# Kernel tuning notes

Hardware: AMD Instinct MI355X
Metric: run time of the kernel (lower is better)

Reference implementation:

```python
import jax, jax.numpy as jnp
import numpy as np

NUM_HEADS = 8


def _mab(Q, K, Wq, bq, Wk, bk, Wv, bv, Wo, bo):
    # MAB with ln=False, dropout=0 (eval). Scale is sqrt(dim_V), matching source.
    B, Lq, _ = Q.shape
    Lk = K.shape[1]
    Dv = Wq.shape[1]
    dh = Dv // NUM_HEADS
    q = (Q @ Wq + bq).reshape(B, Lq, NUM_HEADS, dh).transpose(0, 2, 1, 3)
    k = (K @ Wk + bk).reshape(B, Lk, NUM_HEADS, dh).transpose(0, 2, 1, 3)
    v = (K @ Wv + bv).reshape(B, Lk, NUM_HEADS, dh).transpose(0, 2, 1, 3)
    A = jax.nn.softmax(jnp.einsum('bhqd,bhkd->bhqk', q, k) / jnp.sqrt(jnp.float32(Dv)), axis=-1)
    O = (q + jnp.einsum('bhqk,bhkd->bhqd', A, v)).transpose(0, 2, 1, 3).reshape(B, Lq, Dv)
    return O + jax.nn.relu(O @ Wo + bo)


def _forward(x, adj, gin_W, gin_b, geW1, geb1, geW2, geb2,
             gnW1, gnb1, gnW2, gnb2, goW, gob, S,
             mWq, mbq, mWk, mbk, mWv, mbv, mWo, mbo, finW, finb):
    B, V, T, D = x.shape
    Hd = gin_W.shape[1]
    # --- GNN encoder (adj path) ---
    h = x.reshape(B, V, T * D) @ gin_W + gin_b            # [B,V,H]
    # edge_mlp first linear on cat([h_i,h_j]) == h@Wi (row) + h@Wj (col); avoids 2H concat
    Wi, Wj = geW1[:Hd], geW1[Hd:]
    pre = (h @ Wi)[:, :, None, :] + (h @ Wj)[:, None, :, :] + geb1   # [B,V,V,H]
    e = jax.nn.relu(jax.nn.relu(pre) @ geW2 + geb2)       # [B,V,V,H]
    agg = jnp.einsum('bijh,bij->bih', e, adj)             # mask * sum over j, fused
    node = jax.nn.relu(jax.nn.relu(agg @ gnW1 + gnb1) @ gnW2 + gnb2)
    enc = node @ goW + gob                                # [B,V,H]
    # --- decoder: PMA + SAB + SAB + Linear ---
    o = _mab(jnp.broadcast_to(S, (B,) + S.shape[1:]), enc,
             mWq[0], mbq[0], mWk[0], mbk[0], mWv[0], mbv[0], mWo[0], mbo[0])
    o = _mab(o, o, mWq[1], mbq[1], mWk[1], mbk[1], mWv[1], mbv[1], mWo[1], mbo[1])
    o = _mab(o, o, mWq[2], mbq[2], mWk[2], mbk[2], mWv[2], mbv[2], mWo[2], mbo[2])
    out = o @ finW + finb                                 # [B,num_slots,T*OD]
    return out.reshape(B, S.shape[1], T, finW.shape[1] // T)


def setup_inputs() -> dict:
    key = jax.random.key(0)
    ks = jax.random.split(key, 16)
    B, V, T, D = 4, 256, 12, 4
    H, NS, OD = 256, 16, 32

    def w(k, shape, s=0.02):
        return s * jax.random.normal(k, shape, jnp.float32)

    return {
        'x': jax.random.normal(ks[0], (B, V, T, D), jnp.float32),
        'adj': (jax.random.uniform(ks[1], (B, V, V)) > 0.5).astype(jnp.float32),
        'gin_W': w(ks[2], (T * D, H)), 'gin_b': jnp.zeros((H,), jnp.float32),
        'geW1': w(ks[3], (2 * H, H)), 'geb1': jnp.zeros((H,), jnp.float32),
        'geW2': w(ks[4], (H, H)), 'geb2': jnp.zeros((H,), jnp.float32),
        'gnW1': w(ks[5], (H, H)), 'gnb1': jnp.zeros((H,), jnp.float32),
        'gnW2': w(ks[6], (H, H)), 'gnb2': jnp.zeros((H,), jnp.float32),
        'goW': w(ks[7], (H, H)), 'gob': jnp.zeros((H,), jnp.float32),
        'S': w(ks[8], (1, NS, H), 0.05),
        'mWq': w(ks[9], (3, H, H)), 'mbq': jnp.zeros((3, H), jnp.float32),
        'mWk': w(ks[10], (3, H, H)), 'mbk': jnp.zeros((3, H), jnp.float32),
        'mWv': w(ks[11], (3, H, H)), 'mbv': jnp.zeros((3, H), jnp.float32),
        'mWo': w(ks[12], (3, H, H)), 'mbo': jnp.zeros((3, H), jnp.float32),
        'finW': w(ks[13], (H, T * OD)), 'finb': jnp.zeros((T * OD,), jnp.float32),
    }


def reference(x, adj, gin_W, gin_b, geW1, geb1, geW2, geb2,
              gnW1, gnb1, gnW2, gnb2, goW, gob, S,
              mWq, mbq, mWk, mbk, mWv, mbv, mWo, mbo, finW, finb):
    return _forward(x, adj, gin_W, gin_b, geW1, geb1, geW2, geb2,
                    gnW1, gnb1, gnW2, gnb2, goW, gob, S,
                    mWq, mbq, mWk, mbk, mWv, mbv, mWo, mbo, finW, finb)
```

## Files before the change

kernel.cpp:

```cpp
#include <hip/hip_runtime.h>
#include <hip/hip_bf16.h>

typedef unsigned short u16;
typedef __bf16 bf8v __attribute__((ext_vector_type(8)));
typedef float f4v __attribute__((ext_vector_type(4)));

__device__ __forceinline__ float b2f(u16 v) {
  union { unsigned u; float f; } x; x.u = ((unsigned)v) << 16; return x.f;
}
__device__ __forceinline__ u16 f2b(float f) {
  union { float f; unsigned u; } x; x.f = f;
  unsigned r = (x.u + 0x7FFFu + ((x.u >> 16) & 1u)) >> 16;
  return (u16)r;
}
__device__ __forceinline__ unsigned pkbf(float a, float b) {
  union { __hip_bfloat162 h; unsigned u; } c;
  c.h = __float22bfloat162_rn(make_float2(a, b));
  return c.u;
}
__device__ __forceinline__ void up2(unsigned u, float& lo, float& hi) {
  union { unsigned x; float f; } a, b;
  a.x = u << 16; b.x = u & 0xffff0000u; lo = a.f; hi = b.f;
}

#define NFRAG 19
struct PreArgs {
  const float* fsrc[NFRAG];
  u16* fdst[NFRAG];
  int fstride[NFRAG];
  int fbase[NFRAG + 1];
  int fragTiles, hBase, prepBid, q1Bid;
  const float *x, *ginW, *ginb;
  u16* h_bf;
  const float *mbk, *mbv, *mbq, *S, *mWq;
  float *bkv0, *bqkv1, *bqkv2;
  u16* q1b;
};

__global__ __launch_bounds__(256) void k_pre(PreArgs a) {
  __shared__ u16 ld[256 * 20];
  __shared__ float xs[4][48];
  __shared__ float Ss[4096];
  const int bid = blockIdx.x, t = threadIdx.x;

  if (bid < a.fragTiles) {
    int j = 0;
    while (j + 1 < NFRAG && a.fbase[j + 1] <= bid) j++;
    const int localT = bid - a.fbase[j];
    const float* src = a.fsrc[j];
    const int Ns = a.fstride[j];
    const int n0 = localT * 16;
    {
      const float* s = src + (size_t)t * Ns + n0;
      const float4 v0 = ((const float4*)s)[0], v1 = ((const float4*)s)[1];
      const float4 v2 = ((const float4*)s)[2], v3 = ((const float4*)s)[3];
      unsigned* row = (unsigned*)(ld + t * 20);
      row[0] = pkbf(v0.x, v0.y); row[1] = pkbf(v0.z, v0.w);
      row[2] = pkbf(v1.x, v1.y); row[3] = pkbf(v1.z, v1.w);
      row[4] = pkbf(v2.x, v2.y); row[5] = pkbf(v2.z, v2.w);
      row[6] = pkbf(v3.x, v3.y); row[7] = pkbf(v3.z, v3.w);
    }
    __syncthreads();
    u16* dst = a.fdst[j] + (size_t)localT * 4096;
#pragma unroll
    for (int s2 = 0; s2 < 2; s2++) {
      const int o = t * 2 + s2, kt = o >> 6, lane = o & 63;
      const int nlo = lane & 15, bk = kt * 32 + ((lane >> 4) << 3);
      union { u16 h[8]; uint4 q; } pk;
#pragma unroll
      for (int j2 = 0; j2 < 8; j2++) pk.h[j2] = ld[(bk + j2) * 20 + nlo];
      *(uint4*)(dst + (size_t)(kt * 64 + lane) * 8) = pk.q;
    }
    return;
  }
  if (bid >= a.hBase && bid < a.hBase + 256) {
    const int row0 = (bid - a.hBase) * 4;
    if (t < 192) {
      const int rr = t / 48, k = t % 48;
      xs[rr][k] = a.x[(size_t)(row0 + rr) * 48 + k];
    }
    __syncthreads();
    const float bias = a.ginb[t];
    float acc[4] = {bias, bias, bias, bias};
    for (int k = 0; k < 48; k++) {
      const float w = a.ginW[(size_t)k * 256 + t];
#pragma unroll
      for (int rr = 0; rr < 4; rr++) acc[rr] += xs[rr][k] * w;
    }
#pragma unroll
    for (int rr = 0; rr < 4; rr++) a.h_bf[(size_t)(row0 + rr) * 256 + t] = f2b(acc[rr]);
    return;
  }
  if (bid == a.prepBid) {
    a.bkv0[t] = a.mbk[t]; a.bkv0[256 + t] = a.mbv[t];
    a.bqkv1[t] = a.mbq[256 + t]; a.bqkv1[256 + t] = a.mbk[256 + t]; a.bqkv1[512 + t] = a.mbv[256 + t];
    a.bqkv2[t] = a.mbq[512 + t]; a.bqkv2[256 + t] = a.mbk[512 + t]; a.bqkv2[512 + t] = a.mbv[512 + t];
    return;
  }
  if (bid == a.q1Bid) {
    for (int idx = t; idx < 4096; idx += 256) Ss[idx] = a.S[idx];
    __syncthreads();
    float acc[16];
#pragma unroll
    for (int r = 0; r < 16; r++) acc[r] = 0.f;
    for (int k = 0; k < 256; k++) {
      const float w = a.mWq[(size_t)k * 256 + t];
#pragma unroll
      for (int r = 0; r < 16; r++) acc[r] += Ss[r * 256 + k] * w;
    }
    const float bq = a.mbq[t];
#pragma unroll
    for (int r = 0; r < 16; r++) a.q1b[r * 256 + t] = f2b(acc[r] + bq);
    return;
  }
}

__global__ __launch_bounds__(256) void k_wiwj(
    const u16* __restrict__ h, const u16* __restrict__ frag,
    float* __restrict__ hWiF, u16* __restrict__ hWjB) {
  __shared__ __align__(16) u16 As[64 * 264];
  const int t = threadIdx.x, lane = t & 63, wv = t >> 6;
  const int m0 = blockIdx.x * 64, n0 = blockIdx.y * 128;
  {
    const int row = t >> 2, ch = t & 3;
#pragma unroll
    for (int s = 0; s < 8; s++)
      *(uint4*)(As + row * 264 + ch * 64 + s * 8) =
          *(const uint4*)(h + (size_t)(m0 + row) * 256 + ch * 64 + s * 8);
  }
  __syncthreads();
  f4v acc[4][2];
#pragma unroll
// ... 120 lines not shown
      if (kt < 7) {
#pragma unroll
        for (int nt = 0; nt < 4; nt++) bcur[nt] = bnxt[nt];
      }
    }
    const int rbase = (lane >> 4) * 4;
#pragma unroll
    for (int nt = 0; nt < 4; nt++) {
      float s = 0.f;
#pragma unroll
      for (int jt = 0; jt < 4; jt++) {
        const int r0 = jt * 16 + rbase;
#pragma unroll
        for (int r = 0; r < 4; r++) {
          const float e = fmaxf(acc[jt][nt][r] + bias2[nt], 0.f);
          s += (r0 + r < rows) ? e : 0.f;
        }
      }
      s += __shfl_xor(s, 16);
      s += __shfl_xor(s, 32);
      aggAcc[nt] += s;
    }
    __syncthreads();
  }
  if (lane < 16) {
#pragma unroll
    for (int nt = 0; nt < 4; nt++) {
      const int n = wv * 64 + nt * 16 + lane;
      aggB[(size_t)(b * 256 + i) * 256 + n] = f2b(aggAcc[nt]);
    }
  }
}

#define NBLK 32

__device__ __forceinline__ void gridbar(int* cnt, int gen) {
  __syncthreads();
  if (threadIdx.x == 0) {
    __threadfence();
    __hip_atomic_fetch_add(cnt, 1, __ATOMIC_RELAXED, __HIP_MEMORY_SCOPE_AGENT);
    int it = 0;
    while (__hip_atomic_load(cnt, __ATOMIC_RELAXED, __HIP_MEMORY_SCOPE_AGENT) < NBLK * gen) {
      __builtin_amdgcn_s_sleep(8);
      if (((++it) & 255) == 0)
        __hip_atomic_fetch_add(cnt, 0, __ATOMIC_RELAXED, __HIP_MEMORY_SCOPE_AGENT);
    }
    __threadfence();
  }
  __syncthreads();
}

__device__ void g32(const u16* Al, const u16* frag, const float* bias, int relu,
                    u16* Ol, int t) {
  const int lane = t & 63, wv = t >> 6;
  f4v acc[2][4];
#pragma unroll
  for (int mt = 0; mt < 2; mt++)
#pragma unroll
    for (int nt = 0; nt < 4; nt++) acc[mt][nt] = (f4v){0.f, 0.f, 0.f, 0.f};
#pragma unroll
  for (int kt = 0; kt < 8; kt++) {
    bf8v af[2], bf[4];
#pragma unroll
    for (int mt = 0; mt < 2; mt++)
      af[mt] = *(const bf8v*)(Al + (mt * 16 + (lane & 15)) * 264 + kt * 32 + ((lane >> 4) << 3));
#pragma unroll
    for (int nt = 0; nt < 4; nt++)
      bf[nt] = *(const bf8v*)(frag + ((size_t)((wv * 4 + nt) * 8 + kt) * 64 + lane) * 8);
#pragma unroll
    for (int mt = 0; mt < 2; mt++)
#pragma unroll
      for (int nt = 0; nt < 4; nt++)
        acc[mt][nt] = __builtin_amdgcn_mfma_f32_16x16x32_bf16(af[mt], bf[nt], acc[mt][nt], 0, 0, 0);
  }
#pragma unroll
  for (int mt = 0; mt < 2; mt++)
#pragma unroll
    for (int nt = 0; nt < 4; nt++) {
      const int col = wv * 64 + nt * 16 + (lane & 15);
      const float bv = bias[col];
#pragma unroll
      for (int r = 0; r < 4; r++) {
        const int row = mt * 16 + ((lane >> 4) << 2) + r;
        float v = acc[mt][nt][r] + bv;
// ... 87 lines not shown
#pragma unroll
    for (int q2 = 0; q2 < 4; q2++) { v[q2] = __expf(v[q2] - mx); sum += v[q2]; }
    for (int off = 32; off; off >>= 1) sum += __shfl_xor(sum, off);
    const float inv = 1.f / sum;
#pragma unroll
    for (int q2 = 0; q2 < 4; q2++) sc[r * 256 + lane + q2 * 64] = v[q2] * inv;
  }
  __syncthreads();
  for (int u = t; u < 1024; u += 256) {
    const int row = u >> 2, part = u & 3;
    const uint4 v4 = *(const uint4*)(vbuf + (size_t)(b * Lk + row) * 512 + hd * 32 + part * 8);
    float f0, f1, f2, f3, f4, f5, f6, f7;
    up2(v4.x, f0, f1); up2(v4.y, f2, f3); up2(v4.z, f4, f5); up2(v4.w, f6, f7);
    float4* d = (float4*)(vs + row * 32 + part * 8);
    d[0] = make_float4(f0, f1, f2, f3);
    d[1] = make_float4(f4, f5, f6, f7);
  }
  __syncthreads();
  const int r0 = t >> 5, d = t & 31;
  float a0 = qs[r0 * 32 + d], a1 = qs[(r0 + 8) * 32 + d];
#pragma unroll 4
  for (int j = 0; j < Lk; j++) {
    const float vv = vs[j * 32 + d];
    a0 += sc[r0 * 256 + j] * vv;
    a1 += sc[(r0 + 8) * 256 + j] * vv;
  }
  const int c0 = hd * 32 + d;
  oF[(size_t)(b * 16 + r0) * 256 + c0] = a0;
  oB[(size_t)(b * 16 + r0) * 256 + c0] = f2b(a0);
  oF[(size_t)(b * 16 + r0 + 8) * 256 + c0] = a1;
  oB[(size_t)(b * 16 + r0 + 8) * 256 + c0] = f2b(a1);
}

__device__ void wprojG(const u16* __restrict__ o1b, const float* __restrict__ o1f,
                       const u16* __restrict__ frag, const float* __restrict__ bias,
                       u16* actL, float* residL, int b, int T, int lane) {
  f4v acc = (f4v){0.f, 0.f, 0.f, 0.f};
  const u16* abase = o1b + (size_t)(b * 16 + (lane & 15)) * 256 + ((lane >> 4) << 3);
  const u16* fbase = frag + ((size_t)(T * 8) * 64 + lane) * 8;
#pragma unroll
  for (int kt = 0; kt < 8; kt++)
    acc = __builtin_amdgcn_mfma_f32_16x16x32_bf16(*(const bf8v*)(abase + kt * 32),
                                                  *(const bf8v*)(fbase + (size_t)kt * 512), acc, 0, 0, 0);
  const int col = T * 16 + (lane & 15);
  const float bv = bias[col];
#pragma unroll
  for (int r = 0; r < 4; r++) {
    const int row = ((lane >> 4) << 2) + r;
    const float v = fmaxf(acc[r] + bv, 0.f) + o1f[(size_t)(b * 16 + row) * 256 + col];
    residL[row * 256 + col] = v;
    actL[row * 264 + col] = f2b(v);
  }
}

__device__ void wprojQ(const u16* actL, const u16* __restrict__ frag,
                       const float* __restrict__ bias, u16* qkvL, int T, int lane) {
  f4v acc = (f4v){0.f, 0.f, 0.f, 0.f};
  const u16* abase = actL + (lane & 15) * 264 + ((lane >> 4) << 3);
  const u16* fbase = frag + ((size_t)(T * 8) * 64 + lane) * 8;
#pragma unroll
  for (int kt = 0; kt < 8; kt++)
    acc = __builtin_amdgcn_mfma_f32_16x16x32_bf16(*(const bf8v*)(abase + kt * 32),
                                                  *(const bf8v*)(fbase + (size_t)kt * 512), acc, 0, 0, 0);
  const int col = T * 16 + (lane & 15);
  const float bv = bias[col];
#pragma unroll
  for (int r = 0; r < 4; r++) {
    const int row = ((lane >> 4) << 2) + r;
    qkvL[row * 776 + col] = f2b(acc[r] + bv);
  }
}

__device__ void wprojR(const u16* actIn, const u16* __restrict__ frag,
                       const float* __restrict__ bias, u16* actOut, float* residL,
                       int T, int lane) {
  f4v acc = (f4v){0.f, 0.f, 0.f, 0.f};
  const u16* abase = actIn + (lane & 15) * 264 + ((lane >> 4) << 3);
  const u16* fbase = frag + ((size_t)(T * 8) * 64 + lane) * 8;
#pragma unroll
  for (int kt = 0; kt < 8; kt++)
    acc = __builtin_amdgcn_mfma_f32_16x16x32_bf16(*(const bf8v*)(abase + kt * 32),
                                                  *(const bf8v*)(fbase + (size_t)kt * 512), acc, 0, 0, 0);
  const int col = T * 16 + (lane & 15);
  const float bv = bias[col];
#pragma unroll
  for (int r = 0; r < 4; r++) {
    const int row = ((lane >> 4) << 2) + r;
    const float v = fmaxf(acc[r] + bv, 0.f) + residL[row * 256 + col];
    residL[row * 256 + col] = v;
    actOut[row * 264 + col] = f2b(v);
  }
}

__device__ void wprojF(const u16* actL, const u16* __restrict__ frag,
                       const float* __restrict__ bias, float* __restrict__ outG,
                       int T, int lane) {
  f4v acc = (f4v){0.f, 0.f, 0.f, 0.f};
  const u16* abase = actL + (lane & 15) * 264 + ((lane >> 4) << 3);
  const u16* fbase = frag + ((size_t)(T * 8) * 64 + lane) * 8;
#pragma unroll
  for (int kt = 0; kt < 8; kt++)
    acc = __builtin_amdgcn_mfma_f32_16x16x32_bf16(*(const bf8v*)(abase + kt * 32),
                                                  *(const bf8v*)(fbase + (size_t)kt * 512), acc, 0, 0, 0);
  const int col = T * 16 + (lane & 15);
  const float bv = bias[col];
#pragma unroll
  for (int r = 0; r < 4; r++) {
    const int row = ((lane >> 4) << 2) + r;
    outG[(size_t)row * 384 + col] = acc[r] + bv;
  }
}

__device__ void attnB(const u16* qkvL, float* residL, u16* actOut, float* ps,
                      int hd, int lane) {
  const int r = lane & 15, cg = lane >> 4;
  float qv[32];
  {
    const uint4* qp = (const uint4*)(qkvL + r * 776 + hd * 32);
#pragma unroll
    for (int c4 = 0; c4 < 4; c4++) {
      const uint4 q4 = qp[c4];
      up2(q4.x, qv[c4 * 8 + 0], qv[c4 * 8 + 1]);
      up2(q4.y, qv[c4 * 8 + 2], qv[c4 * 8 + 3]);
      up2(q4.z, qv[c4 * 8 + 4], qv[c4 * 8 + 5]);
      up2(q4.w, qv[c4 * 8 + 6], qv[c4 * 8 + 7]);
    }
  }
  float p[4];
#pragma unroll
  for (int c = 0; c < 4; c++) {
    const int cc = cg * 4 + c;
    const uint4* kp = (const uint4*)(qkvL + cc * 776 + 256 + hd * 32);
    float s = 0.f;
#pragma unroll
    for (int c4 = 0; c4 < 4; c4++) {
      const uint4 k4 = kp[c4];
      float k0, k1;
      up2(k4.x, k0, k1); s += qv[c4 * 8 + 0] * k0 + qv[c4 * 8 + 1] * k1;
      up2(k4.y, k0, k1); s += qv[c4 * 8 + 2] * k0 + qv[c4 * 8 + 3] * k1;
      up2(k4.z, k0, k1); s += qv[c4 * 8 + 4] * k0 + qv[c4 * 8 + 5] * k1;
      up2(k4.w, k0, k1); s += qv[c4 * 8 + 6] * k0 + qv[c4 * 8 + 7] * k1;
    }
    p[c] = s * 0.0625f;
  }
  float mx = fmaxf(fmaxf(p[0], p[1]), fmaxf(p[2], p[3]));
  mx = fmaxf(mx, __shfl_xor(mx, 16));
  mx = fmaxf(mx, __shfl_xor(mx, 32));
  float sum = 0.f;
#pragma unroll
  for (int c = 0; c < 4; c++) { p[c] = __expf(p[c] - mx); sum += p[c]; }
  sum += __shfl_xor(sum, 16);
  sum += __shfl_xor(sum, 32);
  const float inv = 1.f / sum;
#pragma unroll
  for (int c = 0; c < 4; c++) ps[r * 16 + cg * 4 + c] = p[c] * inv;
  float o[8];
#pragma unroll
  for (int j = 0; j < 8; j++) o[j] = qv[cg * 8 + j];
#pragma unroll
  for (int c = 0; c < 16; c++) {
    const float pv = ps[r * 16 + c];
    const uint4 v4 = *(const uint4*)(qkvL + c * 776 + 512 + hd * 32 + cg * 8);
    float v0, v1;
    up2(v4.x, v0, v1); o[0] += pv * v0; o[1] += pv * v1;
    up2(v4.y, v0, v1); o[2] += pv * v0; o[3] += pv * v1;
    up2(v4.z, v0, v1); o[4] += pv * v0; o[5] += pv * v1;
    up2(v4.w, v0, v1); o[6] += pv * v0; o[7] += pv * v1;
  }
  const int col0 = hd * 32 + cg * 8;
#pragma unroll
  for (int j = 0; j < 8; j++) residL[r * 256 + col0 + j] = o[j];
  unsigned* ob = (unsigned*)(actOut + r * 264 + col0);
  ob[0] = pkbf(o[0], o[1]); ob[1] = pkbf(o[2], o[3]);
  ob[2] = pkbf(o[4], o[5]); ob[3] = pkbf(o[6], o[7]);
}

struct TailArgs {
  const u16 *agg, *fGn1, *fGn2, *fGo, *fKV0, *fQKV1, *fQKV2, *fO0, *fO1, *fO2, *fFin, *q1b;
  const float *gnb1, *gnb2, *gob, *bkv0, *bqkv1, *bqkv2, *mbo, *finb;
  u16 *kv1, *o1b;
  float *o1f, *outF;
  int* bar;
};

__global__ __launch_bounds__(256) void k_tail(TailArgs a) {
  __shared__ __align__(16) char smem[62208];
  const int bid = blockIdx.x, t = threadIdx.x;
  const int lane = t & 63, w = t >> 6;

  {
    u16* actA = (u16*)smem;
    u16* actB = (u16*)(smem + 16896);
    const int r0 = bid * 32;
#pragma unroll
    for (int s = 0; s < 4; s++) {
      const int u = t * 4 + s, row = u >> 5, ch = u & 31;
      *(uint4*)(actA + row * 264 + ch * 8) =
          *(const uint4*)(a.agg + (size_t)(r0 + row) * 256 + ch * 8);
    }
    __syncthreads();
    g32(actA, a.fGn1, a.gnb1, 1, actB, t); __syncthreads();
    g32(actB, a.fGn2, a.gnb2, 1, actA, t); __syncthreads();
    g32(actA, a.fGo, a.gob, 0, actB, t); __syncthreads();
    g32kv(actB, a.fKV0, a.bkv0, a.kv1 + (size_t)r0 * 512, t);
  }
  gridbar(a.bar, 1);
  {
    float* qs = (float*)smem;
    float* sc = (float*)(smem + 2048);
    float* vs = (float*)(smem + 18432);
    attn_tile(a.q1b, a.kv1, a.kv1 + 256, a.o1f, a.o1b, bid >> 3, bid & 7, qs, sc, vs, t);
  }
  gridbar(a.bar, 2);
  if (bid >= 4) return;
  {
    const int b = bid;
    u16* act0 = (u16*)smem;
    u16* act1 = (u16*)(smem + 8448);
    u16* qkvL = (u16*)(smem + 16896);
    float* residL = (float*)(smem + 41728);
    float* psL = (float*)(smem + 58112);
    __syncthreads();
    for (int T = w; T < 16; T += 4) wprojG(a.o1b, a.o1f, a.fO0, a.mbo, act0, residL, b, T, lane);
    __syncthreads();
    for (int T = w; T < 48; T += 4) wprojQ(act0, a.fQKV1, a.bqkv1, qkvL, T, lane);
    __syncthreads();
    for (int hd = w; hd < 8; hd += 4) attnB(qkvL, residL, act1, psL + w * 256, hd, lane);
    __syncthreads();
    for (int T = w; T < 16; T += 4) wprojR(act1, a.fO1, a.mbo + 256, act0, residL, T, lane);
    __syncthreads();
    for (int T = w; T < 48; T += 4) wprojQ(act0, a.fQKV2, a.bqkv2, qkvL, T, lane);
    __syncthreads();
    for (int hd = w; hd < 8; hd += 4) attnB(qkvL, residL, act1, psL + w * 256, hd, lane);
    __syncthreads();
    for (int T = w; T < 16; T += 4) wprojR(act1, a.fO2, a.mbo + 512, act0, residL, T, lane);
    __syncthreads();
    for (int T = w; T < 24; T += 4)
      wprojF(act0, a.fFin, a.finb, a.outF + (size_t)b * 16 * 384, T, lane);
  }
}

extern "C" void kernel_launch(void* const* d_in, const int* in_sizes, int n_in,
                              void* d_out, int out_size, void* d_ws, size_t ws_size,
                              hipStream_t stream) {
  const float* x    = (const float*)d_in[0];
  const float* adj  = (const float*)d_in[1];
  const float* ginW = (const float*)d_in[2];
  const float* ginb = (const float*)d_in[3];
  const float* geW1 = (const float*)d_in[4];
  const float* geb1 = (const float*)d_in[5];
  const float* geW2 = (const float*)d_in[6];
  const float* geb2 = (const float*)d_in[7];
  const float* gnW1 = (const float*)d_in[8];
  const float* gnb1 = (const float*)d_in[9];
  const float* gnW2 = (const float*)d_in[10];
  const float* gnb2 = (const float*)d_in[11];
  const float* goW  = (const float*)d_in[12];
  const float* gob  = (const float*)d_in[13];
  const float* S    = (const float*)d_in[14];
  const float* mWq  = (const float*)d_in[15];
  const float* mbq  = (const float*)d_in[16];
  const float* mWk  = (const float*)d_in[17];
  const float* mbk  = (const float*)d_in[18];
  const float* mWv  = (const float*)d_in[19];
  const float* mbv  = (const float*)d_in[20];
  const float* mWo  = (const float*)d_in[21];
  const float* mbo  = (const float*)d_in[22];
  const float* finW = (const float*)d_in[23];
  const float* finb = (const float*)d_in[24];
  (void)in_sizes; (void)n_in; (void)out_size; (void)ws_size;

  char* wp = (char*)d_ws;
  size_t off = 0;
  auto alloc = [&](size_t bytes) -> char* {
    char* p = wp + off;
    off += (bytes + 255) & ~(size_t)255;
    return p;
  };
  u16* h_bf     = (u16*)alloc(1024 * 256 * 2);
  float* hWiF   = (float*)alloc((size_t)1024 * 256 * 4);
  u16* hWjB     = (u16*)alloc(1024 * 256 * 2);
  u16* fWiWj    = (u16*)alloc(512 * 256 * 2);
  u16* fW2      = (u16*)alloc(256 * 256 * 2);
  u16* fGn1     = (u16*)alloc(256 * 256 * 2);
  u16* fGn2     = (u16*)alloc(256 * 256 * 2);
  u16* fGo      = (u16*)alloc(256 * 256 * 2);
  u16* fQ0      = (u16*)alloc(256 * 256 * 2);
  u16* fKV0     = (u16*)alloc(512 * 256 * 2);
  u16* fQKV1    = (u16*)alloc(768 * 256 * 2);
  u16* fQKV2    = (u16*)alloc(768 * 256 * 2);
  u16* fO0      = (u16*)alloc(256 * 256 * 2);
  u16* fO1      = (u16*)alloc(256 * 256 * 2);
  u16* fO2      = (u16*)alloc(256 * 256 * 2);
  u16* fFin     = (u16*)alloc(384 * 256 * 2);
  float* bkv0   = (float*)alloc(512 * 4);
  float* bqkv1  = (float*)alloc(768 * 4);
  float* bqkv2  = (float*)alloc(768 * 4);
  u16* q1b      = (u16*)alloc(16 * 256 * 2);
  u16* agg_b    = (u16*)alloc(1024 * 256 * 2);
  u16* kv1      = (u16*)alloc(1024 * 512 * 2);
  float* o1f    = (float*)alloc(64 * 256 * 4);
  u16* o1b      = (u16*)alloc(64 * 256 * 2);
  int* bar      = (int*)alloc(256);

  PreArgs P{};
  int nj = 0, tiles = 0;
  auto addF = [&](const float* s, int stride, u16* d, int nT) {
    P.fsrc[nj] = s; P.fdst[nj] = d; P.fstride[nj] = stride; P.fbase[nj] = tiles;
    tiles += nT; nj++;
  };
  addF(geW1, 256, fWiWj, 16);
  addF(geW1 + 65536, 256, fWiWj + 16 * 4096, 16);
  addF(geW2, 256, fW2, 16);
  addF(gnW1, 256, fGn1, 16);
  addF(gnW2, 256, fGn2, 16);
  addF(goW, 256, fGo, 16);
  addF(mWq, 256, fQ0, 16);
  addF(mWk, 256, fKV0, 16);
  addF(mWv, 256, fKV0 + 16 * 4096, 16);
  addF(mWq + 65536, 256, fQKV1, 16);
  addF(mWk + 65536, 256, fQKV1 + 16 * 4096, 16);
  addF(mWv + 65536, 256, fQKV1 + 32 * 4096, 16);
  addF(mWq + 131072, 256, fQKV2, 16);
  addF(mWk + 131072, 256, fQKV2 + 16 * 4096, 16);
  addF(mWv + 131072, 256, fQKV2 + 32 * 4096, 16);
  addF(mWo, 256, fO0, 16);
  addF(mWo + 65536, 256, fO1, 16);
  addF(mWo + 131072, 256, fO2, 16);
  addF(finW, 384, fFin, 24);
  P.fbase[nj] = tiles;
  P.fragTiles = tiles;
  P.hBase = tiles;
  P.prepBid = tiles + 256;
  P.q1Bid = tiles + 257;
  P.x = x; P.ginW = ginW; P.ginb = ginb; P.h_bf = h_bf;
  P.mbk = mbk; P.mbv = mbv; P.mbq = mbq; P.S = S; P.mWq = mWq;
  P.bkv0 = bkv0; P.bqkv1 = bqkv1; P.bqkv2 = bqkv2; P.q1b = q1b;

  TailArgs T{};
  T.agg = agg_b; T.fGn1 = fGn1; T.fGn2 = fGn2; T.fGo = fGo; T.fKV0 = fKV0;
  T.fQKV1 = fQKV1; T.fQKV2 = fQKV2; T.fO0 = fO0; T.fO1 = fO1; T.fO2 = fO2;
  T.fFin = fFin; T.q1b = q1b;
  T.gnb1 = gnb1; T.gnb2 = gnb2; T.gob = gob;
  T.bkv0 = bkv0; T.bqkv1 = bqkv1; T.bqkv2 = bqkv2; T.mbo = mbo; T.finb = finb;
  T.kv1 = kv1; T.o1b = o1b; T.o1f = o1f; T.outF = (float*)d_out;
  T.bar = bar;

  hipMemsetAsync(bar, 0, 256, stream);
  k_pre<<<dim3(tiles + 258), dim3(256), 0, stream>>>(P);
  k_wiwj<<<dim3(16, 4), dim3(256), 0, stream>>>(h_bf, fWiWj, hWiF, hWjB);
  k_edge<<<dim3(1024), dim3(256), 0, stream>>>(hWiF, hWjB, adj, geb1, fW2, geb2, agg_b);
  k_tail<<<dim3(NBLK), dim3(256), 0, stream>>>(T);
}
```

Measured before the change: 244.1 us.

## Split tail kernel at grid barriers into three launches and widen decoder blocks

New measurement: 248.9 us. About the same (+2.0%).

```diff
diff --git a/kernel.cpp b/kernel.cpp
--- a/kernel.cpp
+++ b/kernel.cpp
@@ -286,22 +286,6 @@
 
 #define NBLK 32
 
-__device__ __forceinline__ void gridbar(int* cnt, int gen) {
-  __syncthreads();
-  if (threadIdx.x == 0) {
-    __threadfence();
-    __hip_atomic_fetch_add(cnt, 1, __ATOMIC_RELAXED, __HIP_MEMORY_SCOPE_AGENT);
-    int it = 0;
-    while (__hip_atomic_load(cnt, __ATOMIC_RELAXED, __HIP_MEMORY_SCOPE_AGENT) < NBLK * gen) {
-      __builtin_amdgcn_s_sleep(8);
-      if (((++it) & 255) == 0)
-        __hip_atomic_fetch_add(cnt, 0, __ATOMIC_RELAXED, __HIP_MEMORY_SCOPE_AGENT);
-    }
-    __threadfence();
-  }
-  __syncthreads();
-}
-
 __device__ void g32(const u16* Al, const u16* frag, const float* bias, int relu,
                     u16* Ol, int t) {
   const int lane = t & 63, wv = t >> 6;
@@ -455,82 +439,125 @@
   oB[(size_t)(b * 16 + r0 + 8) * 256 + c0] = f2b(a1);
 }
 
-__device__ void wprojG(const u16* __restrict__ o1b, const float* __restrict__ o1f,
-                       const u16* __restrict__ frag, const float* __restrict__ bias,
-                       u16* actL, float* residL, int b, int T, int lane) {
-  f4v acc = (f4v){0.f, 0.f, 0.f, 0.f};
+
+template <int NT>
+__device__ __forceinline__ void wprojGn(
+    const u16* __restrict__ o1b, const float* __restrict__ o1f,
+    const u16* __restrict__ frag, const float* __restrict__ bias,
+    u16* actL, float* residL, int b, int T0, int lane) {
+  f4v acc[NT];
+#pragma unroll
+  for (int nt = 0; nt < NT; nt++) acc[nt] = (f4v){0.f, 0.f, 0.f, 0.f};
   const u16* abase = o1b + (size_t)(b * 16 + (lane & 15)) * 256 + ((lane >> 4) << 3);
-  const u16* fbase = frag + ((size_t)(T * 8) * 64 + lane) * 8;
-#pragma unroll
-  for (int kt = 0; kt < 8; kt++)
-    acc = __builtin_amdgcn_mfma_f32_16x16x32_bf16(*(const bf8v*)(abase + kt * 32),
-                                                  *(const bf8v*)(fbase + (size_t)kt * 512), acc, 0, 0, 0);
-  const int col = T * 16 + (lane & 15);
-  const float bv = bias[col];
-#pragma unroll
-  for (int r = 0; r < 4; r++) {
-    const int row = ((lane >> 4) << 2) + r;
-    const float v = fmaxf(acc[r] + bv, 0.f) + o1f[(size_t)(b * 16 + row) * 256 + col];
-    residL[row * 256 + col] = v;
-    actL[row * 264 + col] = f2b(v);
-  }
-}
-
-__device__ void wprojQ(const u16* actL, const u16* __restrict__ frag,
-                       const float* __restrict__ bias, u16* qkvL, int T, int lane) {
-  f4v acc = (f4v){0.f, 0.f, 0.f, 0.f};
+#pragma unroll
+  for (int kt = 0; kt < 8; kt++) {
+    const bf8v af = *(const bf8v*)(abase + kt * 32);
+#pragma unroll
+    for (int nt = 0; nt < NT; nt++) {
+      const bf8v bf = *(const bf8v*)(frag + ((size_t)((T0 + nt) * 8 + kt) * 64 + lane) * 8);
+      acc[nt] = __builtin_amdgcn_mfma_f32_16x16x32_bf16(af, bf, acc[nt], 0, 0, 0);
+    }
+  }
+#pragma unroll
+  for (int nt = 0; nt < NT; nt++) {
+    const int col = (T0 + nt) * 16 + (lane & 15);
+    const float bv = bias[col];
+#pragma unroll
+    for (int r = 0; r < 4; r++) {
+      const int row = ((lane >> 4) << 2) + r;
+      const float v = fmaxf(acc[nt][r] + bv, 0.f) + o1f[(size_t)(b * 16 + row) * 256 + col];
+      residL[row * 256 + col] = v;
+      actL[row * 264 + col] = f2b(v);
+    }
+  }
+}
+
+template <int NT>
+__device__ __forceinline__ void wprojQn(
+    const u16* actL, const u16* __restrict__ frag,
+    const float* __restrict__ bias, u16* qkvL, int T0, int lane) {
+  f4v acc[NT];
+#pragma unroll
+  for (int nt = 0; nt < NT; nt++) acc[nt] = (f4v){0.f, 0.f, 0.f, 0.f};
   const u16* abase = actL + (lane & 15) * 264 + ((lane >> 4) << 3);
-  const u16* fbase = frag + ((size_t)(T * 8) * 64 + lane) * 8;
-#pragma unroll
-  for (int kt = 0; kt < 8; kt++)
-    acc = __builtin_amdgcn_mfma_f32_16x16x32_bf16(*(const bf8v*)(abase + kt * 32),
-                                                  *(const bf8v*)(fbase + (size_t)kt * 512), acc, 0, 0, 0);
-  const int col = T * 16 + (lane & 15);
-  const float bv = bias[col];
-#pragma unroll
-  for (int r = 0; r < 4; r++) {
-    const int row = ((lane >> 4) << 2) + r;
-    qkvL[row * 776 + col] = f2b(acc[r] + bv);
-  }
-}
-
-__device__ void wprojR(const u16* actIn, const u16* __restrict__ frag,
-                       const float* __restrict__ bias, u16* actOut, float* residL,
-                       int T, int lane) {
-  f4v acc = (f4v){0.f, 0.f, 0.f, 0.f};
+#pragma unroll
+  for (int kt = 0; kt < 8; kt++) {
+    const bf8v af = *(const bf8v*)(abase + kt * 32);
+#pragma unroll
+    for (int nt = 0; nt < NT; nt++) {
+      const bf8v bf = *(const bf8v*)(frag + ((size_t)((T0 + nt) * 8 + kt) * 64 + lane) * 8);
+      acc[nt] = __builtin_amdgcn_mfma_f32_16x16x32_bf16(af, bf, acc[nt], 0, 0, 0);
+    }
+  }
+#pragma unroll
+  for (int nt = 0; nt < NT; nt++) {
+    const int col = (T0 + nt) * 16 + (lane & 15);
+    const float bv = bias[col];
+#pragma unroll
+    for (int r = 0; r < 4; r++) {
+      const int row = ((lane >> 4) << 2) + r;
+      qkvL[row * 776 + col] = f2b(acc[nt][r] + bv);
+    }
+  }
+}
+
+template <int NT>
+__device__ __forceinline__ void wprojRn(
+    const u16* actIn, const u16* __restrict__ frag,
+    const float* __restrict__ bias, u16* actOut, float* residL, int T0, int lane) {
+  f4v acc[NT];
+#pragma unroll
+  for (int nt = 0; nt < NT; nt++) acc[nt] = (f4v){0.f, 0.f, 0.f, 0.f};
   const u16* abase = actIn + (lane & 15) * 264 + ((lane >> 4) << 3);
-  const u16* fbase = frag + ((size_t)(T * 8) * 64 + lane) * 8;
-#pragma unroll
-  for (int kt = 0; kt < 8; kt++)
-    acc = __builtin_amdgcn_mfma_f32_16x16x32_bf16(*(const bf8v*)(abase + kt * 32),
-                                                  *(const bf8v*)(fbase + (size_t)kt * 512), acc, 0, 0, 0);
-  const int col = T * 16 + (lane & 15);
-  const float bv = bias[col];
-#pragma unroll
-  for (int r = 0; r < 4; r++) {
-    const int row = ((lane >> 4) << 2) + r;
-    const float v = fmaxf(acc[r] + bv, 0.f) + residL[row * 256 + col];
-    residL[row * 256 + col] = v;
-    actOut[row * 264 + col] = f2b(v);
-  }
-}
-
-__device__ void wprojF(const u16* actL, const u16* __restrict__ frag,
-                       const float* __restrict__ bias, float* __restrict__ outG,
-                       int T, int lane) {
-  f4v acc = (f4v){0.f, 0.f, 0.f, 0.f};
+#pragma unroll
+  for (int kt = 0; kt < 8; kt++) {
+    const bf8v af = *(const bf8v*)(abase + kt * 32);
+#pragma unroll
+    for (int nt = 0; nt < NT; nt++) {
+      const bf8v bf = *(const bf8v*)(frag + ((size_t)((T0 + nt) * 8 + kt) * 64 + lane) * 8);
+      acc[nt] = __builtin_amdgcn_mfma_f32_16x16x32_bf16(af, bf, acc[nt], 0, 0, 0);
+    }
+  }
+#pragma unroll
+  for (int nt = 0; nt < NT; nt++) {
+    const int col = (T0 + nt) * 16 + (lane & 15);
+    const float bv = bias[col];
+#pragma unroll
+    for (int r = 0; r < 4; r++) {
+      const int row = ((lane >> 4) << 2) + r;
+      const float v = fmaxf(acc[nt][r] + bv, 0.f) + residL[row * 256 + col];
+      residL[row * 256 + col] = v;
+      actOut[row * 264 + col] = f2b(v);
+    }
+  }
+}
+
+template <int NT>
+__device__ __forceinline__ void wprojFn(
+    const u16* actL, const u16* __restrict__ frag,
+    const float* __restrict__ bias, float* __restrict__ outG, int T0, int lane) {
+  f4v acc[NT];
+#pragma unroll
+  for (int nt = 0; nt < NT; nt++) acc[nt] = (f4v){0.f, 0.f, 0.f, 0.f};
   const u16* abase = actL + (lane & 15) * 264 + ((lane >> 4) << 3);
-  const u16* fbase = frag + ((size_t)(T * 8) * 64 + lane) * 8;
-#pragma unroll
-  for (int kt = 0; kt < 8; kt++)
-    acc = __builtin_amdgcn_mfma_f32_16x16x32_bf16(*(const bf8v*)(abase + kt * 32),
-                                                  *(const bf8v*)(fbase + (size_t)kt * 512), acc, 0, 0, 0);
-  const int col = T * 16 + (lane & 15);
-  const float bv = bias[col];
-#pragma unroll
-  for (int r = 0; r < 4; r++) {
-    const int row = ((lane >> 4) << 2) + r;
-    outG[(size_t)row * 384 + col] = acc[r] + bv;
+#pragma unroll
+  for (int kt = 0; kt < 8; kt++) {
+    const bf8v af = *(const bf8v*)(abase + kt * 32);
+#pragma unroll
+    for (int nt = 0; nt < NT; nt++) {
+      const bf8v bf = *(const bf8v*)(frag + ((size_t)((T0 + nt) * 8 + kt) * 64 + lane) * 8);
+      acc[nt] = __builtin_amdgcn_mfma_f32_16x16x32_bf16(af, bf, acc[nt], 0, 0, 0);
+    }
+  }
+#pragma unroll
+  for (int nt = 0; nt < NT; nt++) {
+    const int col = (T0 + nt) * 16 + (lane & 15);
+    const float bv = bias[col];
+#pragma unroll
+    for (int r = 0; r < 4; r++) {
+      const int row = ((lane >> 4) << 2) + r;
+      outG[(size_t)row * 384 + col] = acc[nt][r] + bv;
+    }
   }
 }
 
@@ -603,64 +630,61 @@
   const float *gnb1, *gnb2, *gob, *bkv0, *bqkv1, *bqkv2, *mbo, *finb;
   u16 *kv1, *o1b;
   float *o1f, *outF;
-  int* bar;
 };
 
-__global__ __launch_bounds__(256) void k_tail(TailArgs a) {
-  __shared__ __align__(16) char smem[62208];
+__global__ __launch_bounds__(256) void k_tail1(TailArgs a) {
+  __shared__ __align__(16) char smem[33792];
   const int bid = blockIdx.x, t = threadIdx.x;
-  const int lane = t & 63, w = t >> 6;
-
-  {
-    u16* actA = (u16*)smem;
-    u16* actB = (u16*)(smem + 16896);
-    const int r0 = bid * 32;
-#pragma unroll
-    for (int s = 0; s < 4; s++) {
-      const int u = t * 4 + s, row = u >> 5, ch = u & 31;
-      *(uint4*)(actA + row * 264 + ch * 8) =
-          *(const uint4*)(a.agg + (size_t)(r0 + row) * 256 + ch * 8);
-    }
-    __syncthreads();
-    g32(actA, a.fGn1, a.gnb1, 1, actB, t); __syncthreads();
-    g32(actB, a.fGn2, a.gnb2, 1, actA, t); __syncthreads();
-    g32(actA, a.fGo, a.gob, 0, actB, t); __syncthreads();
-    g32kv(actB, a.fKV0, a.bkv0, a.kv1 + (size_t)r0 * 512, t);
-  }
-  gridbar(a.bar, 1);
-  {
-    float* qs = (float*)smem;
-    float* sc = (float*)(smem + 2048);
-    float* vs = (float*)(smem + 18432);
-    attn_tile(a.q1b, a.kv1, a.kv1 + 256, a.o1f, a.o1b, bid >> 3, bid & 7, qs, sc, vs, t);
-  }
-  gridbar(a.bar, 2);
-  if (bid >= 4) return;
-  {
-    const int b = bid;
-    u16* act0 = (u16*)smem;
-    u16* act1 = (u16*)(smem + 8448);
-    u16* qkvL = (u16*)(smem + 16896);
-    float* residL = (float*)(smem + 41728);
-    float* psL = (float*)(smem + 58112);
-    __syncthreads();
-    for (int T = w; T < 16; T += 4) wprojG(a.o1b, a.o1f, a.fO0, a.mbo, act0, residL, b, T, lane);
-    __syncthreads();
-    for (int T = w; T < 48; T += 4) wprojQ(act0, a.fQKV1, a.bqkv1, qkvL, T, lane);
-    __syncthreads();
-    for (int hd = w; hd < 8; hd += 4) attnB(qkvL, residL, act1, psL + w * 256, hd, lane);
-    __syncthreads();
-    for (int T = w; T < 16; T += 4) wprojR(act1, a.fO1, a.mbo + 256, act0, residL, T, lane);
-    __syncthreads();
-    for (int T = w; T < 48; T += 4) wprojQ(act0, a.fQKV2, a.bqkv2, qkvL, T, lane);
-    __syncthreads();
-    for (int hd = w; hd < 8; hd += 4) attnB(qkvL, residL, act1, psL + w * 256, hd, lane);
-    __syncthreads();
-    for (int T = w; T < 16; T += 4) wprojR(act1, a.fO2, a.mbo + 512, act0, residL, T, lane);
-    __syncthreads();
-    for (int T = w; T < 24; T += 4)
-      wprojF(act0, a.fFin, a.finb, a.outF + (size_t)b * 16 * 384, T, lane);
-  }
+  u16* actA = (u16*)smem;
+  u16* actB = (u16*)(smem + 16896);
+  const int r0 = bid * 32;
+#pragma unroll
+  for (int s = 0; s < 4; s++) {
+    const int u = t * 4 + s, row = u >> 5, ch = u & 31;
+    *(uint4*)(actA + row * 264 + ch * 8) =
+        *(const uint4*)(a.agg + (size_t)(r0 + row) * 256 + ch * 8);
+  }
+  __syncthreads();
+  g32(actA, a.fGn1, a.gnb1, 1, actB, t); __syncthreads();
+  g32(actB, a.fGn2, a.gnb2, 1, actA, t); __syncthreads();
+  g32(actA, a.fGo, a.gob, 0, actB, t); __syncthreads();
+  g32kv(actB, a.fKV0, a.bkv0, a.kv1 + (size_t)r0 * 512, t);
+}
+
+__global__ __launch_bounds__(256) void k_tail2(TailArgs a) {
+  __shared__ __align__(16) char smem[51200];
+  float* qs = (float*)smem;
+  float* sc = (float*)(smem + 2048);
+  float* vs = (float*)(smem + 18432);
+  attn_tile(a.q1b, a.kv1, a.kv1 + 256, a.o1f, a.o1b,
+            (int)(blockIdx.x >> 3), (int)(blockIdx.x & 7), qs, sc, vs, (int)threadIdx.x);
+}
+
+__global__ __launch_bounds__(512) void k_tail3(TailArgs a) {
+  __shared__ __align__(16) char smem[58112];
+  const int t = threadIdx.x, lane = t & 63, w = t >> 6;
+  const int b = blockIdx.x;
+  u16* act0 = (u16*)smem;
+  u16* act1 = (u16*)(smem + 8448);
+  u16* qkvL = (u16*)(smem + 16896);
+  float* residL = (float*)(smem + 41728);
+  float* psL = (float*)smem;
+
+  wprojGn<2>(a.o1b, a.o1f, a.fO0, a.mbo, act0, residL, b, w * 2, lane);
+  __syncthreads();
+  wprojQn<6>(act0, a.fQKV1, a.bqkv1, qkvL, w * 6, lane);
+  __syncthreads();
+  attnB(qkvL, residL, act1, psL + w * 256, w, lane);
+  __syncthreads();
+  wprojRn<2>(act1, a.fO1, a.mbo + 256, act0, residL, w * 2, lane);
+  __syncthreads();
+  wprojQn<6>(act0, a.fQKV2, a.bqkv2, qkvL, w * 6, lane);
+  __syncthreads();
+  attnB(qkvL, residL, act1, psL + w * 256, w, lane);
+  __syncthreads();
+  wprojRn<2>(act1, a.fO2, a.mbo + 512, act0, residL, w * 2, lane);
+  __syncthreads();
+  wprojFn<3>(act0, a.fFin, a.finb, a.outF + (size_t)b * 16 * 384, w * 3, lane);
 }
 
 extern "C" void kernel_launch(void* const* d_in, const int* in_sizes, int n_in,
@@ -724,7 +748,6 @@
   u16* kv1      = (u16*)alloc(1024 * 512 * 2);
   float* o1f    = (float*)alloc(64 * 256 * 4);
   u16* o1b      = (u16*)alloc(64 * 256 * 2);
-  int* bar      = (int*)alloc(256);
 
   PreArgs P{};
   int nj = 0, tiles = 0;
@@ -767,11 +790,11 @@
   T.gnb1 = gnb1; T.gnb2 = gnb2; T.gob = gob;
   T.bkv0 = bkv0; T.bqkv1 = bqkv1; T.bqkv2 = bqkv2; T.mbo = mbo; T.finb = finb;
   T.kv1 = kv1; T.o1b = o1b; T.o1f = o1f; T.outF = (float*)d_out;
-  T.bar = bar;
-
-  hipMemsetAsync(bar, 0, 256, stream);
+
   k_pre<<<dim3(tiles + 258), dim3(256), 0, stream>>>(P);
   k_wiwj<<<dim3(16, 4), dim3(256), 0, stream>>>(h_bf, fWiWj, hWiF, hWjB);
   k_edge<<<dim3(1024), dim3(256), 0, stream>>>(hWiF, hWjB, adj, geb1, fW2, geb2, agg_b);
-  k_tail<<<dim3(NBLK), dim3(256), 0, stream>>>(T);
-}
+  k_tail1<<<dim3(NBLK), dim3(256), 0, stream>>>(T);
+  k_tail2<<<dim3(NBLK), dim3(256), 0, stream>>>(T);
+  k_tail3<<<dim3(4), dim3(512), 0, stream>>>(T);
+}
```

## Spread decoder SAB stages across all tail blocks with grid barriers

Applied to the files above, without the earlier changes.

New measurement: 249.3 us. 1.02x slower.

```diff
diff --git a/kernel.cpp b/kernel.cpp
--- a/kernel.cpp
+++ b/kernel.cpp
@@ -23,7 +23,9 @@
   a.x = u << 16; b.x = u & 0xffff0000u; lo = a.f; hi = b.f;
 }
 
-#define NFRAG 19
+#define NFRAG 18
+#define NBLK 32
+
 struct PreArgs {
   const float* fsrc[NFRAG];
   u16* fdst[NFRAG];
@@ -35,15 +37,15 @@
   const float *mbk, *mbv, *mbq, *S, *mWq;
   float *bkv0, *bqkv1, *bqkv2;
   u16* q1b;
+  int* bar;
 };
 
 __global__ __launch_bounds__(256) void k_pre(PreArgs a) {
-  __shared__ u16 ld[256 * 20];
-  __shared__ float xs[4][48];
-  __shared__ float Ss[4096];
+  __shared__ __align__(16) char smem[27648];
   const int bid = blockIdx.x, t = threadIdx.x;
 
   if (bid < a.fragTiles) {
+    u16* ld = (u16*)smem;
     int j = 0;
     while (j + 1 < NFRAG && a.fbase[j + 1] <= bid) j++;
     const int localT = bid - a.fbase[j];
@@ -73,7 +75,8 @@
     }
     return;
   }
-  if (bid >= a.hBase && bid < a.hBase + 256) {
+  if (bid < a.prepBid) {
+    float (*xs)[48] = (float (*)[48])(smem + 10240);
     const int row0 = (bid - a.hBase) * 4;
     if (t < 192) {
       const int rr = t / 48, k = t % 48;
@@ -92,12 +95,14 @@
     return;
   }
   if (bid == a.prepBid) {
+    if (t < 64) a.bar[t] = 0;
     a.bkv0[t] = a.mbk[t]; a.bkv0[256 + t] = a.mbv[t];
     a.bqkv1[t] = a.mbq[256 + t]; a.bqkv1[256 + t] = a.mbk[256 + t]; a.bqkv1[512 + t] = a.mbv[256 + t];
     a.bqkv2[t] = a.mbq[512 + t]; a.bqkv2[256 + t] = a.mbk[512 + t]; a.bqkv2[512 + t] = a.mbv[512 + t];
     return;
   }
   if (bid == a.q1Bid) {
+    float* Ss = (float*)(smem + 11264);
     for (int idx = t; idx < 4096; idx += 256) Ss[idx] = a.S[idx];
     __syncthreads();
     float acc[16];
@@ -284,20 +289,16 @@
   }
 }
 
-#define NBLK 32
-
 __device__ __forceinline__ void gridbar(int* cnt, int gen) {
   __syncthreads();
   if (threadIdx.x == 0) {
-    __threadfence();
-    __hip_atomic_fetch_add(cnt, 1, __ATOMIC_RELAXED, __HIP_MEMORY_SCOPE_AGENT);
+    __hip_atomic_fetch_add(cnt, 1, __ATOMIC_RELEASE, __HIP_MEMORY_SCOPE_AGENT);
     int it = 0;
-    while (__hip_atomic_load(cnt, __ATOMIC_RELAXED, __HIP_MEMORY_SCOPE_AGENT) < NBLK * gen) {
+    while (__hip_atomic_load(cnt, __ATOMIC_ACQUIRE, __HIP_MEMORY_SCOPE_AGENT) < NBLK * gen) {
       __builtin_amdgcn_s_sleep(8);
       if (((++it) & 255) == 0)
-        __hip_atomic_fetch_add(cnt, 0, __ATOMIC_RELAXED, __HIP_MEMORY_SCOPE_AGENT);
-    }
-    __threadfence();
+        __hip_atomic_fetch_add(cnt, 0, __ATOMIC_ACQ_REL, __HIP_MEMORY_SCOPE_AGENT);
+    }
   }
   __syncthreads();
 }
@@ -455,9 +456,9 @@
   oB[(size_t)(b * 16 + r0 + 8) * 256 + c0] = f2b(a1);
 }
 
-__device__ void wprojG(const u16* __restrict__ o1b, const float* __restrict__ o1f,
-                       const u16* __restrict__ frag, const float* __restrict__ bias,
-                       u16* actL, float* residL, int b, int T, int lane) {
+__device__ void wprojG_g(const u16* __restrict__ o1b, const float* __restrict__ o1f,
+                         const u16* __restrict__ frag, const float* __restrict__ bias,
+                         u16* act, float* resid, int b, int T, int lane) {
   f4v acc = (f4v){0.f, 0.f, 0.f, 0.f};
   const u16* abase = o1b + (size_t)(b * 16 + (lane & 15)) * 256 + ((lane >> 4) << 3);
   const u16* fbase = frag + ((size_t)(T * 8) * 64 + lane) * 8;
@@ -471,15 +472,15 @@
   for (int r = 0; r < 4; r++) {
     const int row = ((lane >> 4) << 2) + r;
     const float v = fmaxf(acc[r] + bv, 0.f) + o1f[(size_t)(b * 16 + row) * 256 + col];
-    residL[row * 256 + col] = v;
-    actL[row * 264 + col] = f2b(v);
-  }
-}
-
-__device__ void wprojQ(const u16* actL, const u16* __restrict__ frag,
-                       const float* __restrict__ bias, u16* qkvL, int T, int lane) {
+    resid[(size_t)(b * 16 + row) * 256 + col] = v;
+    act[(size_t)(b * 16 + row) * 256 + col] = f2b(v);
+  }
+}
+
+__device__ void wprojQ_g(const u16* __restrict__ act, const u16* __restrict__ frag,
+                         const float* __restrict__ bias, u16* qkv, int b, int T, int lane) {
   f4v acc = (f4v){0.f, 0.f, 0.f, 0.f};
-  const u16* abase = actL + (lane & 15) * 264 + ((lane >> 4) << 3);
+  const u16* abase = act + (size_t)(b * 16 + (lane & 15)) * 256 + ((lane >> 4) << 3);
   const u16* fbase = frag + ((size_t)(T * 8) * 64 + lane) * 8;
 #pragma unroll
   for (int kt = 0; kt < 8; kt++)
@@ -490,15 +491,15 @@
 #pragma unroll
   for (int r = 0; r < 4; r++) {
     const int row = ((lane >> 4) << 2) + r;
-    qkvL[row * 776 + col] = f2b(acc[r] + bv);
-  }
-}
-
-__device__ void wprojR(const u16* actIn, const u16* __restrict__ frag,
-                       const float* __restrict__ bias, u16* actOut, float* residL,
-                       int T, int lane) {
+    qkv[(size_t)(b * 16 + row) * 768 + col] = f2b(acc[r] + bv);
+  }
+}
+
+__device__ void wprojR_g(const u16* __restrict__ actIn, const u16* __restrict__ frag,
+                         const float* __restrict__ bias, u16* actOut, float* resid,
+                         int b, int T, int lane) {
   f4v acc = (f4v){0.f, 0.f, 0.f, 0.f};
-  const u16* abase = actIn + (lane & 15) * 264 + ((lane >> 4) << 3);
+  const u16* abase = actIn + (size_t)(b * 16 + (lane & 15)) * 256 + ((lane >> 4) << 3);
   const u16* fbase = frag + ((size_t)(T * 8) * 64 + lane) * 8;
 #pragma unroll
   for (int kt = 0; kt < 8; kt++)
@@ -509,17 +510,17 @@
 #pragma unroll
   for (int r = 0; r < 4; r++) {
     const int row = ((lane >> 4) << 2) + r;
-    const float v = fmaxf(acc[r] + bv, 0.f) + residL[row * 256 + col];
-    residL[row * 256 + col] = v;
-    actOut[row * 264 + col] = f2b(v);
-  }
-}
-
-__device__ void wprojF(const u16* actL, const u16* __restrict__ frag,
-                       const float* __restrict__ bias, float* __restrict__ outG,
-                       int T, int lane) {
+    const float v = fmaxf(acc[r] + bv, 0.f) + resid[(size_t)(b * 16 + row) * 256 + col];
+    resid[(size_t)(b * 16 + row) * 256 + col] = v;
+    actOut[(size_t)(b * 16 + row) * 256 + col] = f2b(v);
+  }
+}
+
+__device__ void wprojF_g(const u16* __restrict__ act, const u16* __restrict__ frag,
+                         const float* __restrict__ bias, float* __restrict__ outF,
+                         int b, int T, int lane) {
   f4v acc = (f4v){0.f, 0.f, 0.f, 0.f};
-  const u16* abase = actL + (lane & 15) * 264 + ((lane >> 4) << 3);
+  const u16* abase = act + (size_t)(b * 16 + (lane & 15)) * 256 + ((lane >> 4) << 3);
   const u16* fbase = frag + ((size_t)(T * 8) * 64 + lane) * 8;
 #pragma unroll
   for (int kt = 0; kt < 8; kt++)
@@ -530,16 +531,16 @@
 #pragma unroll
   for (int r = 0; r < 4; r++) {
     const int row = ((lane >> 4) << 2) + r;
-    outG[(size_t)row * 384 + col] = acc[r] + bv;
-  }
-}
-
-__device__ void attnB(const u16* qkvL, float* residL, u16* actOut, float* ps,
-                      int hd, int lane) {
+    outF[(size_t)(b * 16 + row) * 384 + col] = acc[r] + bv;
+  }
+}
+
+__device__ void attnB_g(const u16* __restrict__ qkv, float* resid, u16* actOut,
+                        float* ps, int b, int hd, int lane) {
   const int r = lane & 15, cg = lane >> 4;
   float qv[32];
   {
-    const uint4* qp = (const uint4*)(qkvL + r * 776 + hd * 32);
+    const uint4* qp = (const uint4*)(qkv + (size_t)(b * 16 + r) * 768 + hd * 32);
 #pragma unroll
     for (int c4 = 0; c4 < 4; c4++) {
       const uint4 q4 = qp[c4];
@@ -553,7 +554,7 @@
 #pragma unroll
   for (int c = 0; c < 4; c++) {
     const int cc = cg * 4 + c;
-    const uint4* kp = (const uint4*)(qkvL + cc * 776 + 256 + hd * 32);
+    const uint4* kp = (const uint4*)(qkv + (size_t)(b * 16 + cc) * 768 + 256 + hd * 32);
     float s = 0.f;
 #pragma unroll
     for (int c4 = 0; c4 < 4; c4++) {
@@ -583,7 +584,7 @@
 #pragma unroll
   for (int c = 0; c < 16; c++) {
     const float pv = ps[r * 16 + c];
-    const uint4 v4 = *(const uint4*)(qkvL + c * 776 + 512 + hd * 32 + cg * 8);
+    const uint4 v4 = *(const uint4*)(qkv + (size_t)(b * 16 + c) * 768 + 512 + hd * 32 + cg * 8);
     float v0, v1;
     up2(v4.x, v0, v1); o[0] += pv * v0; o[1] += pv * v1;
     up2(v4.y, v0, v1); o[2] += pv * v0; o[3] += pv * v1;
@@ -592,8 +593,8 @@
   }
   const int col0 = hd * 32 + cg * 8;
 #pragma unroll
-  for (int j = 0; j < 8; j++) residL[r * 256 + col0 + j] = o[j];
-  unsigned* ob = (unsigned*)(actOut + r * 264 + col0);
+  for (int j = 0; j < 8; j++) resid[(size_t)(b * 16 + r) * 256 + col0 + j] = o[j];
+  unsigned* ob = (unsigned*)(actOut + (size_t)(b * 16 + r) * 256 + col0);
   ob[0] = pkbf(o[0], o[1]); ob[1] = pkbf(o[2], o[3]);
   ob[2] = pkbf(o[4], o[5]); ob[3] = pkbf(o[6], o[7]);
 }
@@ -603,64 +604,59 @@
   const float *gnb1, *gnb2, *gob, *bkv0, *bqkv1, *bqkv2, *mbo, *finb;
   u16 *kv1, *o1b;
   float *o1f, *outF;
+  u16 *act0, *act1, *qkv;
+  float* resid;
   int* bar;
 };
 
-__global__ __launch_bounds__(256) void k_tail(TailArgs a) {
-  __shared__ __align__(16) char smem[62208];
+__device__ void tail1_item(const TailArgs& a, int e, int t, char* smem) {
+  u16* actA = (u16*)smem;
+  u16* actB = (u16*)(smem + 16896);
+  const int r0 = e * 32;
+#pragma unroll
+  for (int s = 0; s < 4; s++) {
+    const int u = t * 4 + s, row = u >> 5, ch = u & 31;
+    *(uint4*)(actA + row * 264 + ch * 8) =
+        *(const uint4*)(a.agg + (size_t)(r0 + row) * 256 + ch * 8);
+  }
+  __syncthreads();
+  g32(actA, a.fGn1, a.gnb1, 1, actB, t); __syncthreads();
+  g32(actB, a.fGn2, a.gnb2, 1, actA, t); __syncthreads();
+  g32(actA, a.fGo, a.gob, 0, actB, t); __syncthreads();
+  g32kv(actB, a.fKV0, a.bkv0, a.kv1 + (size_t)r0 * 512, t);
+}
+
+__device__ void tail2_item(const TailArgs& a, int e, int t, char* smem) {
+  float* qs = (float*)smem;
+  float* sc = (float*)(smem + 2048);
+  float* vs = (float*)(smem + 18432);
+  attn_tile(a.q1b, a.kv1, a.kv1 + 256, a.o1f, a.o1b, e >> 3, e & 7, qs, sc, vs, t);
+}
+
+__global__ __launch_bounds__(256) void k_tailF(TailArgs a) {
+  __shared__ __align__(16) char smem[51200];
   const int bid = blockIdx.x, t = threadIdx.x;
   const int lane = t & 63, w = t >> 6;
 
-  {
-    u16* actA = (u16*)smem;
-    u16* actB = (u16*)(smem + 16896);
-    const int r0 = bid * 32;
-#pragma unroll
-    for (int s = 0; s < 4; s++) {
-      const int u = t * 4 + s, row = u >> 5, ch = u & 31;
-      *(uint4*)(actA + row * 264 + ch * 8) =
-          *(const uint4*)(a.agg + (size_t)(r0 + row) * 256 + ch * 8);
-    }
-    __syncthreads();
-    g32(actA, a.fGn1, a.gnb1, 1, actB, t); __syncthreads();
-    g32(actB, a.fGn2, a.gnb2, 1, actA, t); __syncthreads();
-    g32(actA, a.fGo, a.gob, 0, actB, t); __syncthreads();
-    g32kv(actB, a.fKV0, a.bkv0, a.kv1 + (size_t)r0 * 512, t);
-  }
+  tail1_item(a, bid, t, smem);
   gridbar(a.bar, 1);
-  {
-    float* qs = (float*)smem;
-    float* sc = (float*)(smem + 2048);
-    float* vs = (float*)(smem + 18432);
-    attn_tile(a.q1b, a.kv1, a.kv1 + 256, a.o1f, a.o1b, bid >> 3, bid & 7, qs, sc, vs, t);
-  }
+  tail2_item(a, bid, t, smem);
   gridbar(a.bar, 2);
-  if (bid >= 4) return;
-  {
-    const int b = bid;
-    u16* act0 = (u16*)smem;
-    u16* act1 = (u16*)(smem + 8448);
-    u16* qkvL = (u16*)(smem + 16896);
-    float* residL = (float*)(smem + 41728);
-    float* psL = (float*)(smem + 58112);
-    __syncthreads();
-    for (int T = w; T < 16; T += 4) wprojG(a.o1b, a.o1f, a.fO0, a.mbo, act0, residL, b, T, lane);
-    __syncthreads();
-    for (int T = w; T < 48; T += 4) wprojQ(act0, a.fQKV1, a.bqkv1, qkvL, T, lane);
-    __syncthreads();
-    for (int hd = w; hd < 8; hd += 4) attnB(qkvL, residL, act1, psL + w * 256, hd, lane);
-    __syncthreads();
-    for (int T = w; T < 16; T += 4) wprojR(act1, a.fO1, a.mbo + 256, act0, residL, T, lane);
-    __syncthreads();
-    for (int T = w; T < 48; T += 4) wprojQ(act0, a.fQKV2, a.bqkv2, qkvL, T, lane);
-    __syncthreads();
-    for (int hd = w; hd < 8; hd += 4) attnB(qkvL, residL, act1, psL + w * 256, hd, lane);
-    __syncthreads();
-    for (int T = w; T < 16; T += 4) wprojR(act1, a.fO2, a.mbo + 512, act0, residL, T, lane);
-    __syncthreads();
-    for (int T = w; T < 24; T += 4)
-      wprojF(act0, a.fFin, a.finb, a.outF + (size_t)b * 16 * 384, T, lane);
-  }
+  if (bid < 16) wprojG_g(a.o1b, a.o1f, a.fO0, a.mbo, a.act0, a.resid, w, bid, lane);
+  gridbar(a.bar, 3);
+  for (int T = bid; T < 48; T += 32) wprojQ_g(a.act0, a.fQKV1, a.bqkv1, a.qkv, w, T, lane);
+  gridbar(a.bar, 4);
+  if (w == 0) attnB_g(a.qkv, a.resid, a.act1, (float*)smem, bid >> 3, bid & 7, lane);
+  gridbar(a.bar, 5);
+  if (bid < 16) wprojR_g(a.act1, a.fO1, a.mbo + 256, a.act0, a.resid, w, bid, lane);
+  gridbar(a.bar, 6);
+  for (int T = bid; T < 48; T += 32) wprojQ_g(a.act0, a.fQKV2, a.bqkv2, a.qkv, w, T, lane);
+  gridbar(a.bar, 7);
+  if (w == 0) attnB_g(a.qkv, a.resid, a.act1, (float*)smem, bid >> 3, bid & 7, lane);
+  gridbar(a.bar, 8);
+  if (bid < 16) wprojR_g(a.act1, a.fO2, a.mbo + 512, a.act0, a.resid, w, bid, lane);
+  gridbar(a.bar, 9);
+  if (bid < 24) wprojF_g(a.act0, a.fFin, a.finb, a.outF, w, bid, lane);
 }
 
 extern "C" void kernel_launch(void* const* d_in, const int* in_sizes, int n_in,
@@ -708,7 +704,6 @@
   u16* fGn1     = (u16*)alloc(256 * 256 * 2);
   u16* fGn2     = (u16*)alloc(256 * 256 * 2);
   u16* fGo      = (u16*)alloc(256 * 256 * 2);
-  u16* fQ0      = (u16*)alloc(256 * 256 * 2);
   u16* fKV0     = (u16*)alloc(512 * 256 * 2);
   u16* fQKV1    = (u16*)alloc(768 * 256 * 2);
   u16* fQKV2    = (u16*)alloc(768 * 256 * 2);
@@ -724,6 +719,10 @@
   u16* kv1      = (u16*)alloc(1024 * 512 * 2);
   float* o1f    = (float*)alloc(64 * 256 * 4);
   u16* o1b      = (u16*)alloc(64 * 256 * 2);
+  u16* act0_g   = (u16*)alloc(64 * 256 * 2);
+  u16* act1_g   = (u16*)alloc(64 * 256 * 2);
+  u16* qkv_g    = (u16*)alloc(64 * 768 * 2);
+  float* resid_g= (float*)alloc(64 * 256 * 4);
   int* bar      = (int*)alloc(256);
 
   PreArgs P{};
@@ -738,7 +737,6 @@
   addF(gnW1, 256, fGn1, 16);
   addF(gnW2, 256, fGn2, 16);
   addF(goW, 256, fGo, 16);
-  addF(mWq, 256, fQ0, 16);
   addF(mWk, 256, fKV0, 16);
   addF(mWv, 256, fKV0 + 16 * 4096, 16);
   addF(mWq + 65536, 256, fQKV1, 16);
@@ -759,6 +757,7 @@
   P.x = x; P.ginW = ginW; P.ginb = ginb; P.h_bf = h_bf;
   P.mbk = mbk; P.mbv = mbv; P.mbq = mbq; P.S = S; P.mWq = mWq;
   P.bkv0 = bkv0; P.bqkv1 = bqkv1; P.bqkv2 = bqkv2; P.q1b = q1b;
+  P.bar = bar;
 
   TailArgs T{};
   T.agg = agg_b; T.fGn1 = fGn1; T.fGn2 = fGn2; T.fGo = fGo; T.fKV0 = fKV0;
@@ -767,11 +766,11 @@
   T.gnb1 = gnb1; T.gnb2 = gnb2; T.gob = gob;
   T.bkv0 = bkv0; T.bqkv1 = bqkv1; T.bqkv2 = bqkv2; T.mbo = mbo; T.finb = finb;
   T.kv1 = kv1; T.o1b = o1b; T.o1f = o1f; T.outF = (float*)d_out;
+  T.act0 = act0_g; T.act1 = act1_g; T.qkv = qkv_g; T.resid = resid_g;
   T.bar = bar;
 
-  hipMemsetAsync(bar, 0, 256, stream);
   k_pre<<<dim3(tiles + 258), dim3(256), 0, stream>>>(P);
   k_wiwj<<<dim3(16, 4), dim3(256), 0, stream>>>(h_bf, fWiWj, hWiF, hWjB);
   k_edge<<<dim3(1024), dim3(256), 0, stream>>>(hWiF, hWjB, adj, geb1, fW2, geb2, agg_b);
-  k_tail<<<dim3(NBLK), dim3(256), 0, stream>>>(T);
-}
+  k_tailF<<<dim3(NBLK), dim3(256), 0, stream>>>(T);
+}
```
